# Kernel optimization log

Hardware: AMD Instinct MI355X
Metric: run time of the kernel (lower is better)

## Reference

```python
import jax, jax.numpy as jnp
import numpy as np

B, C_IN, T, DIM_H, HEADS, K = 64, 64, 512, 64, 2, 9
N = B * T            # graph nodes = batch * cycle_size
E = 524288           # edges (avg degree 16)
D = HEADS * DIM_H    # 128, GATv2 concat output
EPS = 1e-5
SLOPE = 0.2          # GATv2 leaky_relu negative slope


def setup_inputs() -> dict:
    key = jax.random.key(0)
    ks = jax.random.split(key, 12)
    s = 0.05
    return {
        'x': jax.random.normal(ks[0], (B, C_IN, T), jnp.float32),
        'edge_index': jax.random.randint(ks[1], (2, E), 0, N, jnp.int32),
        'bn0_g': jnp.ones((C_IN,), jnp.float32),
        'bn0_b': jnp.zeros((C_IN,), jnp.float32),
        'W_l': jax.random.normal(ks[2], (C_IN, D), jnp.float32) * s,
        'W_r': jax.random.normal(ks[3], (C_IN, D), jnp.float32) * s,
        'att': jax.random.normal(ks[4], (HEADS, DIM_H), jnp.float32) * s,
        'gat_b': jnp.zeros((D,), jnp.float32),
        'bn1_g': jnp.ones((D,), jnp.float32),
        'bn1_b': jnp.zeros((D,), jnp.float32),
        'conv_w': jax.random.normal(ks[5], (T, T, K), jnp.float32) * s,
        'conv_b': jnp.zeros((T,), jnp.float32),
        'bn2_g': jnp.ones((T,), jnp.float32),
        'bn2_b': jnp.zeros((T,), jnp.float32),
    }


def _bn(x, g, b, axes, shape):
    # BatchNorm1d in training mode: biased batch stats per channel
    m = jnp.mean(x, axes, keepdims=True)
    v = jnp.var(x, axes, keepdims=True)
    return (x - m) * jax.lax.rsqrt(v + EPS) * g.reshape(shape) + b.reshape(shape)


def _gatv2(x, edge_index, W_l, W_r, att, bias):
    # PyG GATv2Conv: out_i = sum_j softmax_j(att . leaky_relu(xl_j + xr_i)) * xl_j
    xl = (x @ W_l).reshape(N, HEADS, DIM_H)
    xr = (x @ W_r).reshape(N, HEADS, DIM_H)
    loops = jnp.arange(N, dtype=edge_index.dtype)  # add_self_loops=True
    src = jnp.concatenate([edge_index[0], loops])
    dst = jnp.concatenate([edge_index[1], loops])
    h = xl[src] + xr[dst]                       # [E+N, H, dh]
    h = jnp.where(h > 0, h, SLOPE * h)
    logits = jnp.einsum('ehd,hd->eh', h, att)   # [E+N, H]
    mmax = jax.ops.segment_max(logits, dst, num_segments=N)
    a = jnp.exp(logits - mmax[dst])
    z = jax.ops.segment_sum(a, dst, num_segments=N)
    alpha = a / z[dst]                          # scatter-softmax over incoming edges
    out = jax.ops.segment_sum(alpha[:, :, None] * xl[src], dst, num_segments=N)
    return out.reshape(N, D) + bias


def reference(x, edge_index, bn0_g, bn0_b, W_l, W_r, att, gat_b,
              bn1_g, bn1_b, conv_w, conv_b, bn2_g, bn2_b):
    # b0 (batch_size > 1), x: [B, C_IN, T]
    x = _bn(x, bn0_g, bn0_b, (0, 2), (1, C_IN, 1))
    # (skip_connection branch is dead code: its result is overwritten)
    # torch .view on contiguous [B,C,T] -> [B*T, C] == raw reshape
    xn = x.reshape(N, C_IN)
    xn = jax.nn.relu(_bn(_gatv2(xn, edge_index, W_l, W_r, att, gat_b),
                         bn1_g, bn1_b, (0,), (1, D)))
    x3 = xn.reshape(B, D, T)
    residual = x3
    xt = jnp.transpose(x3, (0, 2, 1))           # [B, T, D]: channels=T, length=D
    y = jax.lax.conv_general_dilated(xt, conv_w, (1,), 'SAME',
                                     dimension_numbers=('NCH', 'OIH', 'NCH'))
    y = y + conv_b[None, :, None]
    y = jax.nn.relu(_bn(y, bn2_g, bn2_b, (0, 2), (1, T, 1)))
    y = jnp.transpose(y, (0, 2, 1))             # [B, D, T]
    # dropout(p=0.1) is identity in eval
    return residual + y
```

## Files before the change

kernel.cpp:

```cpp
#include <hip/hip_runtime.h>
#include <stdint.h>

typedef __attribute__((ext_vector_type(8))) __bf16 bf16x8;
typedef __attribute__((ext_vector_type(4))) float f32x4;

#define DEVI __device__ __forceinline__

constexpr int Bn = 64, CIN = 64, Tn = 512, Nn = 32768, Dn = 128;
constexpr int En = 524288, ENn = En + Nn;
constexpr float EPSf = 1e-5f;

constexpr size_t OFF_XL   = 0;
constexpr size_t OFF_XR   = 8388608;
constexpr size_t OFF_GPAD = 16777216;
constexpr size_t OFF_WRE  = 25690112;
constexpr size_t OFF_WT   = 30408704;
constexpr size_t OFF_CNT  = 30441472;
constexpr size_t OFF_STAT = 30572544;
constexpr size_t OFF_SUM0 = OFF_STAT;
constexpr size_t OFF_SQ0  = OFF_STAT + 256;
constexpr size_t OFF_SUM1 = OFF_STAT + 512;
constexpr size_t OFF_SQ1  = OFF_STAT + 4608;
constexpr size_t OFF_SC2  = OFF_STAT + 8704;
constexpr size_t OFF_SH2  = OFF_STAT + 10752;
constexpr size_t OFF_BUCK = OFF_STAT + 12800;
constexpr size_t OFF_Y3   = OFF_BUCK + 8388608;
constexpr size_t WS_NEED  = OFF_Y3 + 8388608;

DEVI float bf2f(unsigned short u){
  union { unsigned int u; float f; } x; x.u = ((unsigned int)u) << 16; return x.f;
}
DEVI unsigned short f2bf(float f){
  union { float f; unsigned int u; } x; x.f = f;
  unsigned int lsb = (x.u >> 16) & 1u;
  return (unsigned short)((x.u + 0x7fffu + lsb) >> 16);
}
DEVI void gl_lds16(const void* g, void* l){
  __builtin_amdgcn_global_load_lds(
      (const __attribute__((address_space(1))) unsigned int*)g,
      (__attribute__((address_space(3))) unsigned int*)l, 16, 0, 0);
}
DEVI float red32(float p){
  p += __shfl_xor(p, 1);  p += __shfl_xor(p, 2);  p += __shfl_xor(p, 4);
  p += __shfl_xor(p, 8);  p += __shfl_xor(p, 16);
  return p;
}
DEVI size_t gpad_addr(int b, int m, int d){
  int ig = m >> 2;
  int chunk = ((m & 3) << 1) | (d >> 6);
  int est = ((d & 63) + ((ig & 7) << 3)) & 63;
  return (size_t)b * 69632 + 2048 + (size_t)ig * 512 + (chunk << 6) + est;
}

__global__ void k_mark(float* out, int n){
  int i = blockIdx.x * 256 + threadIdx.x;
  if (i < n) out[i] = 1.0f;
}

__global__ void __launch_bounds__(256) k_pre(
    const float* __restrict__ x,
    const float* __restrict__ w, const float* __restrict__ wl,
    const float* __restrict__ wr, const int* __restrict__ ei,
    float* __restrict__ sum0, float* __restrict__ sq0,
    unsigned short* __restrict__ wre, unsigned short* __restrict__ wt,
    int* __restrict__ cnt, int* __restrict__ buck){
  __shared__ float l1[256], l2[256];
  int bl = blockIdx.x, t = threadIdx.x;
  if (bl < 256){
    int c = bl >> 2, q = bl & 3;
    const float4* x4 = (const float4*)x;
    float s = 0.f, ss = 0.f;
    #pragma unroll
    for (int j = 0; j < 8; ++j){
      int idx = t + j * 256;
      int b = (q << 4) + (idx >> 7);
      int tt4 = idx & 127;
      float4 v = x4[(size_t)b * 8192 + c * 128 + tt4];
      s  += (v.x + v.y) + (v.z + v.w);
      ss += (v.x * v.x + v.y * v.y) + (v.z * v.z + v.w * v.w);
    }
    l1[t] = s; l2[t] = ss; __syncthreads();
    for (int o = 128; o > 0; o >>= 1){
      if (t < o){ l1[t] += l1[t + o]; l2[t] += l2[t + o]; }
      __syncthreads();
    }
    if (t == 0){
      atomicAdd(sum0 + c, l1[0]);
      atomicAdd(sq0 + c, l2[0]);
    }
  } else if (bl < 772){
    int b2 = bl - 256;
    if (b2 < 512){
      int to = b2;
      size_t rest_to = ((size_t)((to >> 7) * 2 + ((to >> 6) & 1)) << 12)
                     + ((size_t)((to >> 4) & 3) << 9)
                     + ((size_t)(to & 15) << 3);
      for (int it2 = 0; it2 < 2; ++it2){
        int ti = it2 * 256 + t;
        const float* src = w + ((size_t)to * 512 + ti) * 9;
        size_t idx = rest_to
                   + ((size_t)((ti >> 5) & 1) << 11)
                   + ((size_t)((ti >> 3) & 3) << 7)
                   + (size_t)(ti & 7);
        int c = ti >> 6;
        #pragma unroll
        for (int k = 0; k < 9; ++k)
          wre[idx + ((size_t)(k * 8 + c) << 15)] = f2bf(src[k]);
      }
    } else {
      int q = b2 - 512;
      int n = q * 64 + (t >> 2);
      int k0 = (t & 3) * 16;
      for (int k = k0; k < k0 + 16; ++k){
        float v = (n < 128) ? wl[k * 128 + n] : wr[k * 128 + (n - 128)];
        wt[n * 64 + k] = f2bf(v);
      }
    }
  } else {
    int e = (bl - 772) * 256 + t;
    int s, dst;
    if (e < En){ s = ei[e]; dst = ei[En + e]; } else { s = dst = e - En; }
    int slot = atomicAdd(cnt + dst, 1);
    if (slot < 64) buck[dst * 64 + slot] = s;
  }
}

__global__ void __launch_bounds__(256) k_xlxr(
    const float* __restrict__ x, const unsigned short* __restrict__ wt,
    const float* __restrict__ sum0, const float* __restrict__ sq0,
    const float* __restrict__ g0, const float* __restrict__ b0v,
    unsigned short* __restrict__ xl, unsigned short* __restrict__ xr){
  __shared__ unsigned short lA[128 * 64];
  __shared__ unsigned short lB[128 * 64];
  int bl = blockIdx.x, t = threadIdx.x;
  int m0 = (bl & 255) * 128;
  int nt = bl >> 8;
  {
    const unsigned short* gb = wt + nt * 128 * 64;
    #pragma unroll
    for (int i = 0; i < 4; ++i){
      int idx = t + i * 256;
      gl_lds16(gb + idx * 8, &lB[idx * 8]);
    }
  }
  {
    const float4* gx = (const float4*)(x + (size_t)m0 * 64);
    #pragma unroll
    for (int i = 0; i < 8; ++i){
      int idx = t + i * 256;
      float4 v = gx[idx];
      int row = idx >> 4;
      int ch = ((m0 + row) >> 3) & 63;
      float mean = sum0[ch] * (1.f / 32768.f);
      float var  = sq0[ch] * (1.f / 32768.f) - mean * mean;
      float sc = rsqrtf(var + EPSf) * g0[ch];
      float sh = b0v[ch] - mean * sc;
      unsigned int p0 = (unsigned int)f2bf(v.x * sc + sh) | ((unsigned int)f2bf(v.y * sc + sh) << 16);
      unsigned int p1 = (unsigned int)f2bf(v.z * sc + sh) | ((unsigned int)f2bf(v.w * sc + sh) << 16);
      *(uint2*)&lA[idx * 4] = make_uint2(p0, p1);
    }
  }
  __syncthreads();
  int w = t >> 6, lane = t & 63;
  int wm = (w & 1) * 64, wn = (w >> 1) * 64;
  int lrow = lane & 15, quad = lane >> 4;
  const f32x4 fz = {0.f, 0.f, 0.f, 0.f};
  f32x4 acc[4][4];
  #pragma unroll
  for (int i = 0; i < 4; ++i)
    #pragma unroll
    for (int j = 0; j < 4; ++j) acc[i][j] = fz;
  #pragma unroll
  for (int kk = 0; kk < 2; ++kk){
    bf16x8 a[4], bfr[4];
    #pragma unroll
    for (int i = 0; i < 4; ++i){
      a[i]   = *(const bf16x8*)&lA[(wm + i * 16 + lrow) * 64 + kk * 32 + quad * 8];
      bfr[i] = *(const bf16x8*)&lB[(wn + i * 16 + lrow) * 64 + kk * 32 + quad * 8];
    }
    #pragma unroll
    for (int i = 0; i < 4; ++i)
      #pragma unroll
      for (int j = 0; j < 4; ++j)
        acc[i][j] = __builtin_amdgcn_mfma_f32_16x16x32_bf16(a[i], bfr[j], acc[i][j], 0, 0, 0);
  }
  unsigned short* outb = nt ? xr : xl;
  #pragma unroll
  for (int i = 0; i < 4; ++i)
    #pragma unroll
    for (int j = 0; j < 4; ++j)
      #pragma unroll
      for (int r = 0; r < 4; ++r){
        int row = m0 + wm + i * 16 + quad * 4 + r;
        int col = wn + j * 16 + lrow;
        outb[row * 128 + col] = f2bf(acc[i][j][r]);
      }
}

__global__ void __launch_bounds__(256) k_gat(
    const unsigned short* __restrict__ xl, const unsigned short* __restrict__ xr,
    const float* __restrict__ att,
    const int* __restrict__ cnt, const int* __restrict__ buck,
    unsigned short* __restrict__ gpad,
    float* __restrict__ sum1, float* __restrict__ sq1){
  __shared__ float S[4][128], Q[4][128];
  int t = threadIdx.x;
  int wv = t >> 6, lane = t & 63;
  int dst = blockIdx.x * 4 + wv;
  float2 pa = *(const float2*)(att + (lane << 1));
  float a0 = pa.x, a1 = pa.y;
  unsigned int pr = *(const unsigned int*)(xr + (size_t)dst * 128 + (lane << 1));
  float r0 = bf2f((unsigned short)(pr & 0xffffu)), r1 = bf2f((unsigned short)(pr >> 16));
  const int* bk = buck + dst * 64;
  int deg = cnt[dst]; deg = deg > 64 ? 64 : deg;
  float z = 0.f, ac0 = 0.f, ac1 = 0.f;
  int i = 0;
  for (; i + 4 <= deg; i += 4){
    int s0 = bk[i], s1 = bk[i + 1], s2 = bk[i + 2], s3 = bk[i + 3];
    unsigned int px0 = *(const unsigned int*)(xl + (size_t)s0 * 128 + (lane << 1));
    unsigned int px1 = *(const unsigned int*)(xl + (size_t)s1 * 128 + (lane << 1));
    unsigned int px2 = *(const unsigned int*)(xl + (size_t)s2 * 128 + (lane << 1));
    unsigned int px3 = *(const unsigned int*)(xl + (size_t)s3 * 128 + (lane << 1));
    float x00 = bf2f((unsigned short)(px0 & 0xffffu)), x01 = bf2f((unsigned short)(px0 >> 16));
    float x10 = bf2f((unsigned short)(px1 & 0xffffu)), x11 = bf2f((unsigned short)(px1 >> 16));
    float x20 = bf2f((unsigned short)(px2 & 0xffffu)), x21 = bf2f((unsigned short)(px2 >> 16));
    float x30 = bf2f((unsigned short)(px3 & 0xffffu)), x31 = bf2f((unsigned short)(px3 >> 16));
    float h, p0, p1, p2, p3;
    h = x00 + r0; h = fmaxf(h, 0.2f * h); p0 = h * a0;
    h = x01 + r1; h = fmaxf(h, 0.2f * h); p0 += h * a1;
    h = x10 + r0; h = fmaxf(h, 0.2f * h); p1 = h * a0;
    h = x11 + r1; h = fmaxf(h, 0.2f * h); p1 += h * a1;
    h = x20 + r0; h = fmaxf(h, 0.2f * h); p2 = h * a0;
    h = x21 + r1; h = fmaxf(h, 0.2f * h); p2 += h * a1;
    h = x30 + r0; h = fmaxf(h, 0.2f * h); p3 = h * a0;
    h = x31 + r1; h = fmaxf(h, 0.2f * h); p3 += h * a1;
    p0 += __shfl_xor(p0, 1);  p1 += __shfl_xor(p1, 1);
    p2 += __shfl_xor(p2, 1);  p3 += __shfl_xor(p3, 1);
    p0 += __shfl_xor(p0, 2);  p1 += __shfl_xor(p1, 2);
    p2 += __shfl_xor(p2, 2);  p3 += __shfl_xor(p3, 2);
    p0 += __shfl_xor(p0, 4);  p1 += __shfl_xor(p1, 4);
    p2 += __shfl_xor(p2, 4);  p3 += __shfl_xor(p3, 4);
    p0 += __shfl_xor(p0, 8);  p1 += __shfl_xor(p1, 8);
    p2 += __shfl_xor(p2, 8);  p3 += __shfl_xor(p3, 8);
    p0 += __shfl_xor(p0, 16); p1 += __shfl_xor(p1, 16);
    p2 += __shfl_xor(p2, 16); p3 += __shfl_xor(p3, 16);
    float w0 = __expf(p0), w1 = __expf(p1), w2 = __expf(p2), w3 = __expf(p3);
    z += (w0 + w1) + (w2 + w3);
    ac0 += w0 * x00; ac0 += w1 * x10; ac0 += w2 * x20; ac0 += w3 * x30;
    ac1 += w0 * x01; ac1 += w1 * x11; ac1 += w2 * x21; ac1 += w3 * x31;
  }
  for (; i < deg; ++i){
    int s = bk[i];
    unsigned int px = *(const unsigned int*)(xl + (size_t)s * 128 + (lane << 1));
    float x0 = bf2f((unsigned short)(px & 0xffffu)), x1 = bf2f((unsigned short)(px >> 16));
    float h0 = x0 + r0; h0 = fmaxf(h0, 0.2f * h0);
    float h1 = x1 + r1; h1 = fmaxf(h1, 0.2f * h1);
    float p = red32(h0 * a0 + h1 * a1);
    float w = __expf(p);
    z += w; ac0 += w * x0; ac1 += w * x1;
  }
  float inv = (z > 0.f) ? 1.f / z : 0.f;
  float o0 = ac0 * inv, o1 = ac1 * inv;
  size_t off = gpad_addr(dst >> 9, dst & 511, lane << 1);
  *(unsigned int*)(gpad + off) =
      (unsigned int)f2bf(o0) | ((unsigned int)f2bf(o1) << 16);
  S[wv][lane * 2] = o0; S[wv][lane * 2 + 1] = o1;
  Q[wv][lane * 2] = o0 * o0; Q[wv][lane * 2 + 1] = o1 * o1;
  __syncthreads();
  int rep = (blockIdx.x & 7) << 7;
  if (t < 128){
    atomicAdd(sum1 + rep + t, (S[0][t] + S[1][t]) + (S[2][t] + S[3][t]));
  } else {
    int c = t - 128;
    atomicAdd(sq1 + rep + c, (Q[0][c] + Q[1][c]) + (Q[2][c] + Q[3][c]));
  }
}

__global__ void __launch_bounds__(256) k_bn1_apply(
    unsigned short* __restrict__ gpad,
    const float* __restrict__ sums, const float* __restrict__ sumsq,
    const float* __restrict__ g, const float* __restrict__ bb){
  int bl = blockIdx.x, t = threadIdx.x;
  if (bl >= 4096){
    int idx = (bl - 4096) * 256 + t;
    int b = idx >> 10, r = idx & 1023;
    int region = r >> 9, rp = r & 511;
    size_t off = (size_t)b * 69632 + (region ? 67584 : 0) + rp * 4;
    *(uint2*)(gpad + off) = make_uint2(0u, 0u);
    return;
  }
  int gi = bl * 256 + t;
  int f0 = gi * 4;
  int b = f0 >> 16, q = f0 & 65535;
  int m = q >> 7, d0 = q & 127;
  float sc[4], sh[4];
  #pragma unroll
  for (int j = 0; j < 4; ++j){
    int d = d0 + j;
    float s = 0.f, ssq = 0.f;
    #pragma unroll
    for (int r = 0; r < 8; ++r){
      s   += sums[(r << 7) + d];
      ssq += sumsq[(r << 7) + d];
    }
    float mean = s / 32768.f;
    float var  = ssq / 32768.f - mean * mean;
    float rs = rsqrtf(var + EPSf) * g[d];
    sc[j] = rs; sh[j] = bb[d] - mean * rs;
  }
  unsigned short* gp = gpad + gpad_addr(b, m, d0);
  uint2 v = *(const uint2*)gp;
  float o0 = fmaxf(0.f, bf2f((unsigned short)(v.x & 0xffffu)) * sc[0] + sh[0]);
  float o1 = fmaxf(0.f, bf2f((unsigned short)(v.x >> 16))     * sc[1] + sh[1]);
  float o2 = fmaxf(0.f, bf2f((unsigned short)(v.y & 0xffffu)) * sc[2] + sh[2]);
  float o3 = fmaxf(0.f, bf2f((unsigned short)(v.y >> 16))     * sc[3] + sh[3]);
  unsigned int p0 = (unsigned int)f2bf(o0) | ((unsigned int)f2bf(o1) << 16);
  unsigned int p1 = (unsigned int)f2bf(o2) | ((unsigned int)f2bf(o3) << 16);
  *(uint2*)gp = make_uint2(p0, p1);
}

__global__ void __launch_bounds__(256, 4) k_conv(
    const unsigned short* __restrict__ wre,
    const unsigned short* __restrict__ gpad,
    unsigned short* __restrict__ y0, unsigned short* __restrict__ y1,
    unsigned short* __restrict__ y2, unsigned short* __restrict__ y3){
  __shared__ unsigned short lB[2][128 * 64];
  int t = threadIdx.x;
  int id  = blockIdx.x;
  int xcd = id & 7, u = id >> 3;
  int z    = (xcd & 1) * 2 + (u >> 6);
  int b    = (xcd >> 1) * 16 + ((u >> 2) & 15);
  int tile = u & 3;
  int to0  = tile * 128;
  int w = t >> 6, lane = t & 63;
  int wm = (w & 1) * 64, wn = (w >> 1) * 64;
  int mh = w & 1;
  int lrow = lane & 15, quad = lane >> 4;
  const f32x4 fz = {0.f, 0.f, 0.f, 0.f};
  f32x4 acc[4][4];
  #pragma unroll
  for (int i = 0; i < 4; ++i)
    #pragma unroll
    for (int j = 0; j < 4; ++j) acc[i][j] = fz;
  const unsigned short* gbb = gpad + (size_t)b * 69632;
  int og[4], ol[4];
  #pragma unroll
  for (int i = 0; i < 4; ++i){
    int idx = t + i * 256;
    og[i] = (idx >> 3) * 512 + (idx & 7) * 8;
    ol[i] = idx * 8;
  }
  int s0 = z * 18;
  const unsigned short* wlane = wre + ((size_t)((tile << 1) | mh) << 12) + (lane << 3);

  bf16x8 aA[8], aB[8];
  {
    int k0 = s0 >> 3, c0 = s0 & 7;
    const unsigned short* gB = gbb + k0 * 512 + c0 * 64;
    #pragma unroll
    for (int i = 0; i < 4; ++i) gl_lds16(gB + og[i], &lB[0][ol[i]]);
  }
  __builtin_amdgcn_sched_barrier(0);
  #pragma unroll
  for (int f = 0; f < 8; ++f)
    aA[f] = *(const bf16x8*)(wlane + ((size_t)s0 << 15) + (f << 9));
  __builtin_amdgcn_sched_barrier(0);
  {
    int s1 = s0 + 1;
    int k1 = s1 >> 3, c1 = s1 & 7;
    const unsigned short* gB = gbb + k1 * 512 + c1 * 64;
    #pragma unroll
    for (int i = 0; i < 4; ++i) gl_lds16(gB + og[i], &lB[1][ol[i]]);
  }
  __builtin_amdgcn_sched_barrier(0);

#define STEP(IT, AC, AN) do {                                              \
    int it_ = (IT);                                                        \
    int cb_ = it_ & 1;                                                     \
    int s_  = s0 + it_;                                                    \
    if (it_ < 17) { asm volatile("s_waitcnt vmcnt(4)" ::: "memory"); }     \
    else          { asm volatile("s_waitcnt vmcnt(0)" ::: "memory"); }     \
    __builtin_amdgcn_sched_barrier(0);                                     \
    __builtin_amdgcn_s_barrier();                                          \
    __builtin_amdgcn_sched_barrier(0);                                     \
    {                                                                      \
      int k_ = s_ >> 3;                                                    \
      int rb_ = (k_ + 4 + lrow) & 7;                                       \
      const unsigned short* lb_ = lB[cb_];                                 \
      _Pragma("unroll")                                                    \
      for (int kk = 0; kk < 2; ++kk){                                      \
        int colB = ((kk << 5) + (quad << 3) + (rb_ << 3)) & 63;            \
        bf16x8 bfr[4];                                                     \
        _Pragma("unroll")                                                  \
        for (int j = 0; j < 4; ++j)                                        \
          bfr[j] = *(const bf16x8*)&lb_[(wn + j * 16 + lrow) * 64 + colB]; \
        _Pragma("unroll")                                                  \
        for (int i = 0; i < 4; ++i)                                        \
          _Pragma("unroll")                                                \
          for (int j = 0; j < 4; ++j)                                      \
            acc[i][j] = __builtin_amdgcn_mfma_f32_16x16x32_bf16(           \
                AC[kk * 4 + i], bfr[j], acc[i][j], 0, 0, 0);               \
        __builtin_amdgcn_sched_barrier(0);                                 \
      }                                                                    \
    }                                                                      \
    if (it_ < 17){                                                         \
      _Pragma("unroll")                                                    \
      for (int f = 0; f < 8; ++f)                                          \
        AN[f] = *(const bf16x8*)(wlane + ((size_t)(s_ + 1) << 15) + (f << 9)); \
    }                                                                      \
    __builtin_amdgcn_sched_barrier(0);                                     \
    __builtin_amdgcn_s_barrier();                                          \
    if (it_ < 16){                                                         \
      int sn_ = s_ + 2;                                                    \
      int kn_ = sn_ >> 3, cn_ = sn_ & 7;                                   \
      const unsigned short* gB_ = gbb + kn_ * 512 + cn_ * 64;              \
      _Pragma("unroll")                                                    \
      for (int i = 0; i < 4; ++i) gl_lds16(gB_ + og[i], &lB[cb_][ol[i]]);  \
    }                                                                      \
    __builtin_amdgcn_sched_barrier(0);                                     \
  } while (0)

  for (int it2 = 0; it2 < 9; ++it2){
    STEP(2 * it2,     aA, aB);
    STEP(2 * it2 + 1, aB, aA);
  }
#undef STEP

  unsigned short* yo = (z & 2) ? ((z & 1) ? y3 : y2) : ((z & 1) ? y1 : y0);
  #pragma unroll
  for (int i = 0; i < 4; ++i)
    #pragma unroll
    for (int j = 0; j < 4; ++j)
      #pragma unroll
      for (int r = 0; r < 4; ++r){
        int to = to0 + wm + i * 16 + quad * 4 + r;
        int p  = wn + j * 16 + lrow;
        yo[((size_t)b * 512 + to) * 128 + p] = f2bf(acc[i][j][r]);
      }
}

__global__ void k_bn2_stats(const unsigned short* __restrict__ y0,
                            const unsigned short* __restrict__ y1,
                            const unsigned short* __restrict__ y2,
                            const unsigned short* __restrict__ y3,
                            const float* __restrict__ g, const float* __restrict__ bb,
                            float* __restrict__ scale, float* __restrict__ shift){
  int to = blockIdx.x, t = threadIdx.x;
  int p = t & 127, b0 = t >> 7;
  float s = 0.f, ss = 0.f;
  for (int b = b0; b < 64; b += 2){
    size_t idx = ((size_t)b * 512 + to) * 128 + p;
    float v = (bf2f(y0[idx]) + bf2f(y1[idx])) + (bf2f(y2[idx]) + bf2f(y3[idx]));
    s += v; ss += v * v;
  }
  __shared__ float l1[256], l2[256];
  l1[t] = s; l2[t] = ss; __syncthreads();
  for (int o = 128; o > 0; o >>= 1){
    if (t < o){ l1[t] += l1[t + o]; l2[t] += l2[t + o]; }
    __syncthreads();
  }
  if (t == 0){
    float mean = l1[0] / 8192.f;
    float var  = l2[0] / 8192.f - mean * mean;
    float rs = rsqrtf(var + EPSf) * g[to];
    scale[to] = rs;
    shift[to] = bb[to] - mean * rs;
  }
}

__global__ void __launch_bounds__(256) k_final(
    const unsigned short* __restrict__ y0, const unsigned short* __restrict__ y1,
    const unsigned short* __restrict__ y2, const unsigned short* __restrict__ y3,
    const unsigned short* __restrict__ gpad,
    const float* __restrict__ scale, const float* __restrict__ shift,
    float* __restrict__ out){
  __shared__ float lt[32][33];
  int jt = blockIdx.x, it = blockIdx.y, b = blockIdx.z;
  int j0 = jt * 32, i0 = it * 32;
  int t = threadIdx.x;
  #pragma unroll
  for (int q = 0; q < 4; ++q){
    int li = t + q * 256;
    int r = li >> 5, cc = li & 31;
    int j = j0 + r;
    size_t idx = ((size_t)b * 512 + j) * 128 + i0 + cc;
    float v = (bf2f(y0[idx]) + bf2f(y1[idx])) + (bf2f(y2[idx]) + bf2f(y3[idx]));
    lt[r][cc] = fmaxf(0.f, v * scale[j] + shift[j]);
  }
  __syncthreads();
  const unsigned short* gbb = gpad + (size_t)b * 69632 + 2048;
  #pragma unroll
  for (int q = 0; q < 4; ++q){
    int li = t + q * 256;
    int ii = li >> 5, jj = li & 31;
    int i = i0 + ii, j = j0 + jj;
    int est = ((j & 63) + ((i & 7) << 3)) & 63;
    float res = bf2f(gbb[(size_t)i * 512 + ((j >> 6) << 6) + est]);
    size_t o = (size_t)b * 65536 + (size_t)i * 512 + j;
    out[o] = res + lt[jj][ii];
  }
}

extern "C" void kernel_launch(void* const* d_in, const int* in_sizes, int n_in,
                              void* d_out, int out_size, void* d_ws, size_t ws_size,
                              hipStream_t stream){
  const float* x     = (const float*)d_in[0];
  const int*   ei    = (const int*)d_in[1];
  const float* bn0g  = (const float*)d_in[2];
  const float* bn0b  = (const float*)d_in[3];
  const float* Wl    = (const float*)d_in[4];
  const float* Wr    = (const float*)d_in[5];
  const float* att   = (const float*)d_in[6];
  const float* bn1g  = (const float*)d_in[8];
  const float* bn1b  = (const float*)d_in[9];
  const float* convw = (const float*)d_in[10];
  const float* bn2g  = (const float*)d_in[12];
  const float* bn2b  = (const float*)d_in[13];
  float* out = (float*)d_out;

  if (ws_size < WS_NEED){
    k_mark<<<(out_size + 255) / 256, 256, 0, stream>>>(out, out_size);
    return;
  }
  char* ws = (char*)d_ws;
  unsigned short* xl   = (unsigned short*)(ws + OFF_XL);
  unsigned short* xr   = (unsigned short*)(ws + OFF_XR);
  unsigned short* y0   = (unsigned short*)(ws + OFF_XL);
  unsigned short* y1   = (unsigned short*)(ws + OFF_XR);
  unsigned short* y2   = (unsigned short*)(ws + OFF_BUCK);
  unsigned short* y3   = (unsigned short*)(ws + OFF_Y3);
  unsigned short* gpad = (unsigned short*)(ws + OFF_GPAD);
  unsigned short* wre  = (unsigned short*)(ws + OFF_WRE);
  unsigned short* wt   = (unsigned short*)(ws + OFF_WT);
  int*            cnt  = (int*)(ws + OFF_CNT);
  int*            buck = (int*)(ws + OFF_BUCK);
  float*          sum0 = (float*)(ws + OFF_SUM0);
  float*          sq0  = (float*)(ws + OFF_SQ0);
  float*          sum1 = (float*)(ws + OFF_SUM1);
  float*          sq1  = (float*)(ws + OFF_SQ1);
  float*          sc2  = (float*)(ws + OFF_SC2);
  float*          sh2  = (float*)(ws + OFF_SH2);

  hipMemsetAsync(cnt, 0, 139776, stream);

  k_pre<<<2948, 256, 0, stream>>>(x, convw, Wl, Wr, ei, sum0, sq0, wre, wt, cnt, buck);
  k_xlxr<<<512, 256, 0, stream>>>(x, wt, sum0, sq0, bn0g, bn0b, xl, xr);
  k_gat<<<8192, 256, 0, stream>>>(xl, xr, att, cnt, buck, gpad, sum1, sq1);
  k_bn1_apply<<<4352, 256, 0, stream>>>(gpad, sum1, sq1, bn1g, bn1b);
  k_conv<<<1024, 256, 0, stream>>>(wre, gpad, y0, y1, y2, y3);
  k_bn2_stats<<<512, 256, 0, stream>>>(y0, y1, y2, y3, bn2g, bn2b, sc2, sh2);
  k_final<<<dim3(16, 4, 64), 256, 0, stream>>>(y0, y1, y2, y3, gpad, sc2, sh2, out);

  (void)in_sizes; (void)n_in;
}
```

Baseline: 278.4 us.

## Halve conv split-K to two partials with triple-buffered LDS pipeline

The conv kernel's K-split drops from four partial outputs to two, so each block runs 36 reduction steps instead of 18 and the grid shrinks from 1024 to 512 blocks. The B-tile LDS ring grows from two to three buffers, letting the next tile's global-to-LDS load be issued right after the barrier and removing the second barrier per step. Downstream stats and final kernels read two partial buffers instead of four, which cuts partial-sum traffic and workspace. The trade-off is fewer blocks, which may underfill the GPU's CUs, and more LDS per block with the occupancy hint removed from launch_bounds.

```diff
diff --git a/kernel.cpp b/kernel.cpp
--- a/kernel.cpp
+++ b/kernel.cpp
@@ -24,8 +24,7 @@
 constexpr size_t OFF_SC2  = OFF_STAT + 8704;
 constexpr size_t OFF_SH2  = OFF_STAT + 10752;
 constexpr size_t OFF_BUCK = OFF_STAT + 12800;
-constexpr size_t OFF_Y3   = OFF_BUCK + 8388608;
-constexpr size_t WS_NEED  = OFF_Y3 + 8388608;
+constexpr size_t WS_NEED  = OFF_BUCK + 8388608;
 
 DEVI float bf2f(unsigned short u){
   union { unsigned int u; float f; } x; x.u = ((unsigned int)u) << 16; return x.f;
@@ -319,17 +318,16 @@
   *(uint2*)gp = make_uint2(p0, p1);
 }
 
-__global__ void __launch_bounds__(256, 4) k_conv(
+__global__ void __launch_bounds__(256) k_conv(
     const unsigned short* __restrict__ wre,
     const unsigned short* __restrict__ gpad,
-    unsigned short* __restrict__ y0, unsigned short* __restrict__ y1,
-    unsigned short* __restrict__ y2, unsigned short* __restrict__ y3){
-  __shared__ unsigned short lB[2][128 * 64];
+    unsigned short* __restrict__ y0, unsigned short* __restrict__ y1){
+  __shared__ unsigned short lB[3][128 * 64];
   int t = threadIdx.x;
   int id  = blockIdx.x;
   int xcd = id & 7, u = id >> 3;
-  int z    = (xcd & 1) * 2 + (u >> 6);
-  int b    = (xcd >> 1) * 16 + ((u >> 2) & 15);
+  int z    = xcd & 1;
+  int b    = (xcd >> 1) * 16 + (u >> 2);
   int tile = u & 3;
   int to0  = tile * 128;
   int w = t >> 6, lane = t & 63;
@@ -350,7 +348,7 @@
     og[i] = (idx >> 3) * 512 + (idx & 7) * 8;
     ol[i] = idx * 8;
   }
-  int s0 = z * 18;
+  int s0 = z * 36;
   const unsigned short* wlane = wre + ((size_t)((tile << 1) | mh) << 12) + (lane << 3);
 
   bf16x8 aA[8], aB[8];
@@ -373,20 +371,31 @@
     for (int i = 0; i < 4; ++i) gl_lds16(gB + og[i], &lB[1][ol[i]]);
   }
   __builtin_amdgcn_sched_barrier(0);
-
-#define STEP(IT, AC, AN) do {                                              \
+  #pragma unroll
+  for (int f = 0; f < 8; ++f)
+    aB[f] = *(const bf16x8*)(wlane + ((size_t)(s0 + 1) << 15) + (f << 9));
+  __builtin_amdgcn_sched_barrier(0);
+
+#define STEP(IT, RD, WR, A_) do {                                          \
     int it_ = (IT);                                                        \
-    int cb_ = it_ & 1;                                                     \
     int s_  = s0 + it_;                                                    \
-    if (it_ < 17) { asm volatile("s_waitcnt vmcnt(4)" ::: "memory"); }     \
+    if (it_ < 35) { asm volatile("s_waitcnt vmcnt(12)" ::: "memory"); }    \
     else          { asm volatile("s_waitcnt vmcnt(0)" ::: "memory"); }     \
     __builtin_amdgcn_sched_barrier(0);                                     \
     __builtin_amdgcn_s_barrier();                                          \
     __builtin_amdgcn_sched_barrier(0);                                     \
+    if (it_ < 34){                                                         \
+      int sn_ = s_ + 2;                                                    \
+      int kn_ = sn_ >> 3, cn_ = sn_ & 7;                                   \
+      const unsigned short* gB_ = gbb + kn_ * 512 + cn_ * 64;              \
+      _Pragma("unroll")                                                    \
+      for (int i = 0; i < 4; ++i) gl_lds16(gB_ + og[i], &lB[WR][ol[i]]);   \
+    }                                                                      \
+    __builtin_amdgcn_sched_barrier(0);                                     \
     {                                                                      \
       int k_ = s_ >> 3;                                                    \
       int rb_ = (k_ + 4 + lrow) & 7;                                       \
-      const unsigned short* lb_ = lB[cb_];                                 \
+      const unsigned short* lb_ = lB[RD];                                  \
       _Pragma("unroll")                                                    \
       for (int kk = 0; kk < 2; ++kk){                                      \
         int colB = ((kk << 5) + (quad << 3) + (rb_ << 3)) & 63;            \
@@ -399,34 +408,29 @@
           _Pragma("unroll")                                                \
           for (int j = 0; j < 4; ++j)                                      \
             acc[i][j] = __builtin_amdgcn_mfma_f32_16x16x32_bf16(           \
-                AC[kk * 4 + i], bfr[j], acc[i][j], 0, 0, 0);               \
-        __builtin_amdgcn_sched_barrier(0);                                 \
+                A_[kk * 4 + i], bfr[j], acc[i][j], 0, 0, 0);               \
       }                                                                    \
     }                                                                      \
-    if (it_ < 17){                                                         \
+    __builtin_amdgcn_sched_barrier(0);                                     \
+    if (it_ < 34){                                                         \
       _Pragma("unroll")                                                    \
       for (int f = 0; f < 8; ++f)                                          \
-        AN[f] = *(const bf16x8*)(wlane + ((size_t)(s_ + 1) << 15) + (f << 9)); \
-    }                                                                      \
-    __builtin_amdgcn_sched_barrier(0);                                     \
-    __builtin_amdgcn_s_barrier();                                          \
-    if (it_ < 16){                                                         \
-      int sn_ = s_ + 2;                                                    \
-      int kn_ = sn_ >> 3, cn_ = sn_ & 7;                                   \
-      const unsigned short* gB_ = gbb + kn_ * 512 + cn_ * 64;              \
-      _Pragma("unroll")                                                    \
-      for (int i = 0; i < 4; ++i) gl_lds16(gB_ + og[i], &lB[cb_][ol[i]]);  \
+        A_[f] = *(const bf16x8*)(wlane + ((size_t)(s_ + 2) << 15) + (f << 9)); \
     }                                                                      \
     __builtin_amdgcn_sched_barrier(0);                                     \
   } while (0)
 
-  for (int it2 = 0; it2 < 9; ++it2){
-    STEP(2 * it2,     aA, aB);
-    STEP(2 * it2 + 1, aB, aA);
+  for (int g = 0; g < 6; ++g){
+    STEP(g * 6 + 0, 0, 2, aA);
+    STEP(g * 6 + 1, 1, 0, aB);
+    STEP(g * 6 + 2, 2, 1, aA);
+    STEP(g * 6 + 3, 0, 2, aB);
+    STEP(g * 6 + 4, 1, 0, aA);
+    STEP(g * 6 + 5, 2, 1, aB);
   }
 #undef STEP
 
-  unsigned short* yo = (z & 2) ? ((z & 1) ? y3 : y2) : ((z & 1) ? y1 : y0);
+  unsigned short* yo = z ? y1 : y0;
   #pragma unroll
   for (int i = 0; i < 4; ++i)
     #pragma unroll
@@ -441,8 +445,6 @@
 
 __global__ void k_bn2_stats(const unsigned short* __restrict__ y0,
                             const unsigned short* __restrict__ y1,
-                            const unsigned short* __restrict__ y2,
-                            const unsigned short* __restrict__ y3,
                             const float* __restrict__ g, const float* __restrict__ bb,
                             float* __restrict__ scale, float* __restrict__ shift){
   int to = blockIdx.x, t = threadIdx.x;
@@ -450,7 +452,7 @@
   float s = 0.f, ss = 0.f;
   for (int b = b0; b < 64; b += 2){
     size_t idx = ((size_t)b * 512 + to) * 128 + p;
-    float v = (bf2f(y0[idx]) + bf2f(y1[idx])) + (bf2f(y2[idx]) + bf2f(y3[idx]));
+    float v = bf2f(y0[idx]) + bf2f(y1[idx]);
     s += v; ss += v * v;
   }
   __shared__ float l1[256], l2[256];
@@ -470,7 +472,6 @@
 
 __global__ void __launch_bounds__(256) k_final(
     const unsigned short* __restrict__ y0, const unsigned short* __restrict__ y1,
-    const unsigned short* __restrict__ y2, const unsigned short* __restrict__ y3,
     const unsigned short* __restrict__ gpad,
     const float* __restrict__ scale, const float* __restrict__ shift,
     float* __restrict__ out){
@@ -484,7 +485,7 @@
     int r = li >> 5, cc = li & 31;
     int j = j0 + r;
     size_t idx = ((size_t)b * 512 + j) * 128 + i0 + cc;
-    float v = (bf2f(y0[idx]) + bf2f(y1[idx])) + (bf2f(y2[idx]) + bf2f(y3[idx]));
+    float v = bf2f(y0[idx]) + bf2f(y1[idx]);
     lt[r][cc] = fmaxf(0.f, v * scale[j] + shift[j]);
   }
   __syncthreads();
@@ -527,8 +528,6 @@
   unsigned short* xr   = (unsigned short*)(ws + OFF_XR);
   unsigned short* y0   = (unsigned short*)(ws + OFF_XL);
   unsigned short* y1   = (unsigned short*)(ws + OFF_XR);
-  unsigned short* y2   = (unsigned short*)(ws + OFF_BUCK);
-  unsigned short* y3   = (unsigned short*)(ws + OFF_Y3);
   unsigned short* gpad = (unsigned short*)(ws + OFF_GPAD);
   unsigned short* wre  = (unsigned short*)(ws + OFF_WRE);
   unsigned short* wt   = (unsigned short*)(ws + OFF_WT);
@@ -547,9 +546,9 @@
   k_xlxr<<<512, 256, 0, stream>>>(x, wt, sum0, sq0, bn0g, bn0b, xl, xr);
   k_gat<<<8192, 256, 0, stream>>>(xl, xr, att, cnt, buck, gpad, sum1, sq1);
   k_bn1_apply<<<4352, 256, 0, stream>>>(gpad, sum1, sq1, bn1g, bn1b);
-  k_conv<<<1024, 256, 0, stream>>>(wre, gpad, y0, y1, y2, y3);
-  k_bn2_stats<<<512, 256, 0, stream>>>(y0, y1, y2, y3, bn2g, bn2b, sc2, sh2);
-  k_final<<<dim3(16, 4, 64), 256, 0, stream>>>(y0, y1, y2, y3, gpad, sc2, sh2, out);
+  k_conv<<<512, 256, 0, stream>>>(wre, gpad, y0, y1);
+  k_bn2_stats<<<512, 256, 0, stream>>>(y0, y1, bn2g, bn2b, sc2, sh2);
+  k_final<<<dim3(16, 4, 64), 256, 0, stream>>>(y0, y1, gpad, sc2, sh2, out);
 
   (void)in_sizes; (void)n_in;
 }
```

Result: faster. 258.2 us (-7.3%).
